# Kernel tuning notes

Measured on AMD Instinct MI355X. Metric: run time of the kernel, lower is better.

## Reference

```python
import jax, jax.numpy as jnp
import numpy as np

B, T, DQ, DM, D, F, K, WIN = 64, 2000, 1024, 512, 128, 32, 31, 7
NEG = -2.0**32 + 1.0

def setup_inputs() -> dict:
    key = jax.random.key(0)
    ks = jax.random.split(key, 12)
    return {
        "query": jax.random.normal(ks[0], (B, DQ), jnp.float32),
        "memory": jax.random.normal(ks[1], (B, T, DM), jnp.float32),
        "prev_alignments": jax.random.uniform(ks[2], (B, T), jnp.float32),
        "prev_max_attentions": jax.random.randint(ks[3], (B,), 0, T),
        "memory_lengths": jax.random.randint(ks[4], (B,), T // 2, T),
        "Wq": jax.random.normal(ks[5], (DQ, D), jnp.float32) * 0.02,
        "Wm": jax.random.normal(ks[6], (DM, D), jnp.float32) * 0.02,
        "conv_kernel": jax.random.normal(ks[7], (K, 1, F), jnp.float32) * 0.1,
        "conv_bias": jnp.zeros((F,), jnp.float32),
        "Wloc": jax.random.normal(ks[8], (F, D), jnp.float32) * 0.1,
        "score_v": jax.random.normal(ks[9], (D,), jnp.float32) * 0.1,
        "score_b": jnp.zeros((D,), jnp.float32),
    }

def reference(query, memory, prev_alignments, prev_max_attentions, memory_lengths,
              Wq, Wm, conv_kernel, conv_bias, Wloc, score_v, score_b):
    # projections
    pq = (query @ Wq)[:, None, :]                              # [B,1,D]
    values = jnp.einsum('btm,md->btd', memory, Wm)             # [B,T,D]
    # location features: Conv1D 'same' over prev alignments
    f = jax.lax.conv_general_dilated(
        prev_alignments[:, :, None], conv_kernel, (1,), 'SAME',
        dimension_numbers=('NWC', 'WIO', 'NWC')) + conv_bias    # [B,T,F]
    ploc = jnp.einsum('btf,fd->btd', f, Wloc)                  # [B,T,D]
    # additive energy
    energy = jnp.sum(score_v * jnp.tanh(values + pq + ploc + score_b), axis=2)  # [B,T]
    # monotonic window mask + length mask
    t_idx = jnp.arange(T)
    key_mask = t_idx[None, :] < prev_max_attentions[:, None]
    mask_lengths = jnp.maximum(0, T - WIN - prev_max_attentions)
    reverse_mask = (t_idx[None, :] < mask_lengths[:, None])[:, ::-1]
    length_mask = t_idx[None, :] < memory_lengths[:, None]
    mask = (~(key_mask | reverse_mask)) & length_mask
    energy = jnp.where(mask, energy, NEG)
    alignments = jax.nn.softmax(energy, axis=1)                # [B,T]
    max_attentions = jnp.argmax(alignments, axis=1)            # [B]
    attention = jnp.einsum('bt,btd->bd', alignments, values)   # [B,D]
    next_state = alignments + prev_alignments                  # cumulate_weight=True
    return attention, alignments, next_state, max_attentions
```

## Files before the change

### kernel.cpp

```cpp
#include <hip/hip_runtime.h>

#define B    64
#define T    2000
#define DQ   1024
#define DM   512
#define D    128
#define F    32
#define KK   31
#define WIN  7
#define NCH  32
#define CH   63
#define NCS  (B * NCH)
#define NPQ  (B * 4)

#define PQ4_OFF (NCS * DM)

#define OUT_ALIGN 8192
#define OUT_NEXT  (8192 + B*T)
#define OUT_ARG   (8192 + 2*B*T)

__global__ void __launch_bounds__(512)
K1(const float* __restrict__ q, const float* __restrict__ mem,
   const int* __restrict__ pm, const int* __restrict__ ml,
   const float* __restrict__ Wq, float* __restrict__ part,
   float* __restrict__ pq4) {
    __shared__ float red[4][D];
    int blk = blockIdx.x;
    int tid = threadIdx.x;

    if (blk < NCS) {
        int b = blk >> 5, c = blk & 31;
        if (pm[b] < ml[b]) return;
        int t0 = c * CH, t1 = t0 + CH;
        if (t1 > T) t1 = T;
        const float* mp = mem + ((size_t)b * T + t0) * DM + tid;
        float a0 = 0.f, a1 = 0.f, a2 = 0.f, a3 = 0.f;
        int t = t0;
        for (; t + 4 <= t1; t += 4) {
            a0 += mp[0];
            a1 += mp[DM];
            a2 += mp[2 * DM];
            a3 += mp[3 * DM];
            mp += 4 * (size_t)DM;
        }
        for (; t < t1; ++t) { a0 += *mp; mp += DM; }
        part[((size_t)b * NCH + c) * DM + tid] = ((a0 + a1) + (a2 + a3)) * (1.f / (float)T);
        return;
    }

    int s = blk - NCS;
    int b = s >> 2, j = s & 3;
    int d = tid & 127, kk = tid >> 7;
    int k0 = j * 256 + kk * 64;
    const float* qp = q + (size_t)b * DQ + k0;
    const float* wp = Wq + (size_t)k0 * D + d;
    float acc = 0.f;
    #pragma unroll 4
    for (int k = 0; k < 64; ++k)
        acc += qp[k] * wp[(size_t)k * D];
    red[kk][d] = acc;
    __syncthreads();
    if (tid < D)
        pq4[((size_t)b * 4 + j) * D + tid] =
            (red[0][tid] + red[1][tid]) + (red[2][tid] + red[3][tid]);
}

__global__ void __launch_bounds__(512)
K2(const float* __restrict__ q, const float* __restrict__ mem,
   const float* __restrict__ pa, const int* __restrict__ pm, const int* __restrict__ ml,
   const float* __restrict__ Wq, const float* __restrict__ Wm,
   const float* __restrict__ ck, const float* __restrict__ cb,
   const float* __restrict__ Wloc, const float* __restrict__ sv,
   const float* __restrict__ sb, const float* __restrict__ part,
   const float* __restrict__ pq4, float* __restrict__ out, int lowmem) {
    __shared__ __align__(16) float mrow[WIN][DM];
    __shared__ float fsh[WIN][F];
    __shared__ float2 pacc2[WIN][8][64];
    __shared__ float vsh[WIN][D];
    __shared__ float pqs[D];
    __shared__ float esh[WIN];
    __shared__ float ash[WIN];
    __shared__ int   sbest;

    int b = blockIdx.x;
    int tid = threadIdx.x;
    int lane = tid & 63;
    int wave = tid >> 6;
    int p = pm[b], L = ml[b];
    int wstart = p, wlen = 0;
    if (p < L) { int we = p + WIN; if (we > L) we = L; wlen = we - p; }

    if (wlen > 0) {
        for (int e = tid; e < WIN * DM; e += 512) {
            int i = e >> 9, m = e & 511;
            mrow[i][m] = (i < wlen) ? mem[((size_t)b * T + wstart + i) * DM + m] : 0.f;
        }
        if (tid < WIN * F) {
            int i = tid >> 5, f = tid & 31;
            if (i < wlen) {
                int t = wstart + i;
                float acc = cb[f];
                for (int k = 0; k < KK; ++k) {
                    int tt = t + k - 15;
                    float x = (tt >= 0 && tt < T) ? pa[(size_t)b * T + tt] : 0.f;
                    acc += x * ck[k * F + f];
                }
                fsh[i][f] = acc;
            } else if (i < WIN) {
                fsh[i][f] = 0.f;
            }
        }
        if (!lowmem) {
            if (tid < D) {
                const float* pp = pq4 + (size_t)b * 4 * D;
                pqs[tid] = (pp[tid] + pp[D + tid]) + (pp[2 * D + tid] + pp[3 * D + tid]) + sb[tid];
            }
        } else {
            int d = tid & 127, j = tid >> 7;
            int k0 = j * 256;
            const float* qp = q + (size_t)b * DQ + k0;
            float acc = 0.f;
            for (int k = 0; k < 256; ++k)
                acc += qp[k] * Wq[(size_t)(k0 + k) * D + d];
            ((float*)pacc2)[j * D + d] = acc;
            __syncthreads();
            if (tid < D) {
                const float* pp = (const float*)pacc2;
                pqs[tid] = (pp[tid] + pp[D + tid]) + (pp[2 * D + tid] + pp[3 * D + tid]) + sb[tid];
            }
        }
        __syncthreads();

        {
            const float2* Wm2 = (const float2*)Wm;
            float2 acc[WIN];
            #pragma unroll
            for (int i = 0; i < WIN; ++i) { acc[i].x = 0.f; acc[i].y = 0.f; }
            int m0 = wave * 64;
            for (int mm = 0; mm < 64; ++mm) {
                int m = m0 + mm;
                float2 wrow = Wm2[(size_t)m * 64 + lane];
                #pragma unroll
                for (int i = 0; i < WIN; ++i) {
                    float a = mrow[i][m];
                    acc[i].x += a * wrow.x;
                    acc[i].y += a * wrow.y;
                }
            }
            #pragma unroll
            for (int i = 0; i < WIN; ++i) pacc2[i][wave][lane] = acc[i];
        }
        __syncthreads();

        if (wave < wlen) {
            int i = wave;
            float2 s2 = {0.f, 0.f};
            #pragma unroll
            for (int w = 0; w < 8; ++w) {
                s2.x += pacc2[i][w][lane].x;
                s2.y += pacc2[i][w][lane].y;
            }
            ((float2*)vsh[i])[lane] = s2;
            const float2* Wl2 = (const float2*)Wloc;
            float p0 = 0.f, p1 = 0.f;
            #pragma unroll
            for (int f = 0; f < F; ++f) {
                float fv = fsh[i][f];
                float2 wv = Wl2[f * 64 + lane];
                p0 += fv * wv.x; p1 += fv * wv.y;
            }
            int c0 = 2 * lane, c1 = c0 + 1;
            float x = sv[c0] * tanhf(s2.x + pqs[c0] + p0)
                    + sv[c1] * tanhf(s2.y + pqs[c1] + p1);
            for (int o = 32; o > 0; o >>= 1) x += __shfl_xor(x, o);
            if (lane == 0) esh[i] = x;
        }
        __syncthreads();

        if (tid == 0) {
            float a[WIN];
            int best = 0;
            float mx = esh[0];
            for (int i = 1; i < wlen; ++i) if (esh[i] > mx) mx = esh[i];
            float s = 0.f;
            for (int i = 0; i < wlen; ++i) { a[i] = expf(esh[i] - mx); s += a[i]; }
            float inv = 1.f / s;
            float ab = -1.f;
            for (int i = 0; i < wlen; ++i) {
                a[i] *= inv;
                if (a[i] > ab) { ab = a[i]; best = i; }
            }
            for (int i = 0; i < WIN; ++i) ash[i] = (i < wlen) ? a[i] : 0.f;
            sbest = wstart + best;
        }
        __syncthreads();

        if (tid < D) {
            float a = 0.f;
            for (int i = 0; i < wlen; ++i) a += ash[i] * vsh[i][tid];
            out[b * D + tid] = a;
        }
    } else {
        float* ctxs = (float*)mrow;
        float* gpart = ((float*)mrow) + DM;
        if (!lowmem) {
            float s = 0.f;
            #pragma unroll 8
            for (int cc = 0; cc < NCH; ++cc)
                s += part[((size_t)b * NCH + cc) * DM + tid];
            ctxs[tid] = s;
        } else {
            const float* mp = mem + (size_t)b * T * DM + tid;
            float a0 = 0.f, a1 = 0.f, a2 = 0.f, a3 = 0.f;
            int t = 0;
            for (; t + 4 <= T; t += 4) {
                a0 += mp[0]; a1 += mp[DM]; a2 += mp[2 * DM]; a3 += mp[3 * DM];
                mp += 4 * (size_t)DM;
            }
            for (; t < T; ++t) { a0 += *mp; mp += DM; }
            ctxs[tid] = ((a0 + a1) + (a2 + a3)) * (1.f / (float)T);
        }
        __syncthreads();
        {
            int col = tid & 127, j = tid >> 7;
            const float* wp = Wm + (size_t)(j * 128) * D + col;
            float acc = 0.f;
            for (int mm = 0; mm < 128; ++mm)
                acc += ctxs[j * 128 + mm] * wp[(size_t)mm * D];
            gpart[j * D + col] = acc;
        }
        __syncthreads();
        if (tid < D)
            out[b * D + tid] = gpart[tid] + gpart[D + tid] + gpart[2 * D + tid] + gpart[3 * D + tid];
    }

    {
        float invT = 1.f / (float)T;
        for (int t = tid; t < T; t += 512) {
            float a;
            if (wlen == 0) a = invT;
            else a = (t >= wstart && t < wstart + wlen) ? ash[t - wstart] : 0.f;
            out[OUT_ALIGN + b * T + t] = a;
            out[OUT_NEXT + b * T + t] = pa[(size_t)b * T + t] + a;
        }
        if (tid == 0) out[OUT_ARG + b] = (float)((wlen > 0) ? sbest : 0);
    }
}

extern "C" void kernel_launch(void* const* d_in, const int* in_sizes, int n_in,
                              void* d_out, int out_size, void* d_ws, size_t ws_size,
                              hipStream_t stream) {
    const float* query = (const float*)d_in[0];
    const float* memory = (const float*)d_in[1];
    const float* prev_align = (const float*)d_in[2];
    const int* prev_max = (const int*)d_in[3];
    const int* mem_len = (const int*)d_in[4];
    const float* Wq = (const float*)d_in[5];
    const float* Wm = (const float*)d_in[6];
    const float* ck = (const float*)d_in[7];
    const float* cb = (const float*)d_in[8];
    const float* Wloc = (const float*)d_in[9];
    const float* sv = (const float*)d_in[10];
    const float* sb = (const float*)d_in[11];
    float* out = (float*)d_out;

    float* part = (float*)d_ws;
    float* pq4 = (float*)d_ws + PQ4_OFF;

    size_t need = (size_t)(NCS * DM + NPQ * D) * 4;
    int lowmem = (ws_size < need) ? 1 : 0;

    if (!lowmem)
        K1<<<NCS + NPQ, 512, 0, stream>>>(query, memory, prev_max, mem_len,
                                          Wq, part, pq4);
    K2<<<B, 512, 0, stream>>>(query, memory, prev_align, prev_max, mem_len,
                              Wq, Wm, ck, cb, Wloc, sv, sb,
                              part, pq4, out, lowmem);
}
```

Before: 30.95 us.

## Move window memory projection into first kernel to shorten serial second kernel

The 7-row window projection against Wm (memory rows times Wm) moves out of the per-batch K2 blocks into 64 extra K1 blocks. Each of those blocks writes per-wave partial sums to workspace, and K2 then sums them. The aim is to shorten K2, which runs only 64 blocks and serially loads memory rows and does the GEMV, by overlapping that work with the mean-reduction blocks already in K1. The low-workspace path is split into a separate K2L kernel. In exchange the change needs more workspace and adds global partial-sum traffic, and K1 also grows its shared memory, which may lower its occupancy.

Result: faster. 27.41 us (median of 2 runs) (-11.4%).

```diff
diff --git a/kernel.cpp b/kernel.cpp
--- a/kernel.cpp
+++ b/kernel.cpp
@@ -14,6 +14,7 @@
 #define NPQ  (B * 4)
 
 #define PQ4_OFF (NCS * DM)
+#define VP_OFF  (NCS * DM + NPQ * D)
 
 #define OUT_ALIGN 8192
 #define OUT_NEXT  (8192 + B*T)
@@ -22,9 +23,10 @@
 __global__ void __launch_bounds__(512)
 K1(const float* __restrict__ q, const float* __restrict__ mem,
    const int* __restrict__ pm, const int* __restrict__ ml,
-   const float* __restrict__ Wq, float* __restrict__ part,
-   float* __restrict__ pq4) {
+   const float* __restrict__ Wq, const float* __restrict__ Wm,
+   float* __restrict__ part, float* __restrict__ pq4, float* __restrict__ vpart) {
     __shared__ float red[4][D];
+    __shared__ __align__(16) float mrow[WIN][DM];
     int blk = blockIdx.x;
     int tid = threadIdx.x;
 
@@ -48,7 +50,40 @@
         return;
     }
 
-    int s = blk - NCS;
+    if (blk < NCS + B) {
+        int b = blk - NCS;
+        int p = pm[b], L = ml[b];
+        int wstart = p, wlen = 0;
+        if (p < L) { int we = p + WIN; if (we > L) we = L; wlen = we - p; }
+        if (wlen == 0) return;
+        for (int e = tid; e < WIN * DM; e += 512) {
+            int i = e >> 9, m = e & 511;
+            mrow[i][m] = (i < wlen) ? mem[((size_t)b * T + wstart + i) * DM + m] : 0.f;
+        }
+        __syncthreads();
+        int lane = tid & 63, wave = tid >> 6;
+        const float2* Wm2 = (const float2*)Wm;
+        float2 acc[WIN];
+        #pragma unroll
+        for (int i = 0; i < WIN; ++i) { acc[i].x = 0.f; acc[i].y = 0.f; }
+        int m0 = wave * 64;
+        for (int mm = 0; mm < 64; ++mm) {
+            int m = m0 + mm;
+            float2 wrow = Wm2[(size_t)m * 64 + lane];
+            #pragma unroll
+            for (int i = 0; i < WIN; ++i) {
+                float a = mrow[i][m];
+                acc[i].x += a * wrow.x;
+                acc[i].y += a * wrow.y;
+            }
+        }
+        float2* vp = (float2*)vpart + ((size_t)b * 8 + wave) * (WIN * 64);
+        #pragma unroll
+        for (int i = 0; i < WIN; ++i) vp[i * 64 + lane] = acc[i];
+        return;
+    }
+
+    int s = blk - NCS - B;
     int b = s >> 2, j = s & 3;
     int d = tid & 127, kk = tid >> 7;
     int k0 = j * 256 + kk * 64;
@@ -66,21 +101,18 @@
 }
 
 __global__ void __launch_bounds__(512)
-K2(const float* __restrict__ q, const float* __restrict__ mem,
-   const float* __restrict__ pa, const int* __restrict__ pm, const int* __restrict__ ml,
-   const float* __restrict__ Wq, const float* __restrict__ Wm,
-   const float* __restrict__ ck, const float* __restrict__ cb,
-   const float* __restrict__ Wloc, const float* __restrict__ sv,
-   const float* __restrict__ sb, const float* __restrict__ part,
-   const float* __restrict__ pq4, float* __restrict__ out, int lowmem) {
-    __shared__ __align__(16) float mrow[WIN][DM];
+K2(const float* __restrict__ pa, const int* __restrict__ pm, const int* __restrict__ ml,
+   const float* __restrict__ Wm, const float* __restrict__ ck, const float* __restrict__ cb,
+   const float* __restrict__ Wloc, const float* __restrict__ sv, const float* __restrict__ sb,
+   const float* __restrict__ part, const float* __restrict__ pq4,
+   const float* __restrict__ vpart, float* __restrict__ out) {
     __shared__ float fsh[WIN][F];
-    __shared__ float2 pacc2[WIN][8][64];
     __shared__ float vsh[WIN][D];
     __shared__ float pqs[D];
     __shared__ float esh[WIN];
     __shared__ float ash[WIN];
     __shared__ int   sbest;
+    __shared__ __align__(16) float cg[DM + 4 * D];
 
     int b = blockIdx.x;
     int tid = threadIdx.x;
@@ -91,10 +123,6 @@
     if (p < L) { int we = p + WIN; if (we > L) we = L; wlen = we - p; }
 
     if (wlen > 0) {
-        for (int e = tid; e < WIN * DM; e += 512) {
-            int i = e >> 9, m = e & 511;
-            mrow[i][m] = (i < wlen) ? mem[((size_t)b * T + wstart + i) * DM + m] : 0.f;
-        }
         if (tid < WIN * F) {
             int i = tid >> 5, f = tid & 31;
             if (i < wlen) {
@@ -110,55 +138,21 @@
                 fsh[i][f] = 0.f;
             }
         }
-        if (!lowmem) {
-            if (tid < D) {
-                const float* pp = pq4 + (size_t)b * 4 * D;
-                pqs[tid] = (pp[tid] + pp[D + tid]) + (pp[2 * D + tid] + pp[3 * D + tid]) + sb[tid];
-            }
-        } else {
-            int d = tid & 127, j = tid >> 7;
-            int k0 = j * 256;
-            const float* qp = q + (size_t)b * DQ + k0;
-            float acc = 0.f;
-            for (int k = 0; k < 256; ++k)
-                acc += qp[k] * Wq[(size_t)(k0 + k) * D + d];
-            ((float*)pacc2)[j * D + d] = acc;
-            __syncthreads();
-            if (tid < D) {
-                const float* pp = (const float*)pacc2;
-                pqs[tid] = (pp[tid] + pp[D + tid]) + (pp[2 * D + tid] + pp[3 * D + tid]) + sb[tid];
-            }
-        }
-        __syncthreads();
-
-        {
-            const float2* Wm2 = (const float2*)Wm;
-            float2 acc[WIN];
-            #pragma unroll
-            for (int i = 0; i < WIN; ++i) { acc[i].x = 0.f; acc[i].y = 0.f; }
-            int m0 = wave * 64;
-            for (int mm = 0; mm < 64; ++mm) {
-                int m = m0 + mm;
-                float2 wrow = Wm2[(size_t)m * 64 + lane];
-                #pragma unroll
-                for (int i = 0; i < WIN; ++i) {
-                    float a = mrow[i][m];
-                    acc[i].x += a * wrow.x;
-                    acc[i].y += a * wrow.y;
-                }
-            }
-            #pragma unroll
-            for (int i = 0; i < WIN; ++i) pacc2[i][wave][lane] = acc[i];
+        if (tid < D) {
+            const float* pp = pq4 + (size_t)b * 4 * D;
+            pqs[tid] = (pp[tid] + pp[D + tid]) + (pp[2 * D + tid] + pp[3 * D + tid]) + sb[tid];
         }
         __syncthreads();
 
         if (wave < wlen) {
             int i = wave;
+            const float2* vp = (const float2*)vpart + (size_t)b * 8 * (WIN * 64);
             float2 s2 = {0.f, 0.f};
             #pragma unroll
             for (int w = 0; w < 8; ++w) {
-                s2.x += pacc2[i][w][lane].x;
-                s2.y += pacc2[i][w][lane].y;
+                float2 v = vp[(size_t)w * (WIN * 64) + i * 64 + lane];
+                s2.x += v.x;
+                s2.y += v.y;
             }
             ((float2*)vsh[i])[lane] = s2;
             const float2* Wl2 = (const float2*)Wloc;
@@ -201,25 +195,177 @@
             out[b * D + tid] = a;
         }
     } else {
+        float* ctxs = cg;
+        float* gpart = cg + DM;
+        float s = 0.f;
+        #pragma unroll 8
+        for (int cc = 0; cc < NCH; ++cc)
+            s += part[((size_t)b * NCH + cc) * DM + tid];
+        ctxs[tid] = s;
+        __syncthreads();
+        {
+            int col = tid & 127, j = tid >> 7;
+            const float* wp = Wm + (size_t)(j * 128) * D + col;
+            float acc = 0.f;
+            for (int mm = 0; mm < 128; ++mm)
+                acc += ctxs[j * 128 + mm] * wp[(size_t)mm * D];
+            gpart[j * D + col] = acc;
+        }
+        __syncthreads();
+        if (tid < D)
+            out[b * D + tid] = gpart[tid] + gpart[D + tid] + gpart[2 * D + tid] + gpart[3 * D + tid];
+    }
+
+    {
+        float invT = 1.f / (float)T;
+        for (int t = tid; t < T; t += 512) {
+            float a;
+            if (wlen == 0) a = invT;
+            else a = (t >= wstart && t < wstart + wlen) ? ash[t - wstart] : 0.f;
+            out[OUT_ALIGN + b * T + t] = a;
+            out[OUT_NEXT + b * T + t] = pa[(size_t)b * T + t] + a;
+        }
+        if (tid == 0) out[OUT_ARG + b] = (float)((wlen > 0) ? sbest : 0);
+    }
+}
+
+__global__ void __launch_bounds__(512)
+K2L(const float* __restrict__ q, const float* __restrict__ mem,
+    const float* __restrict__ pa, const int* __restrict__ pm, const int* __restrict__ ml,
+    const float* __restrict__ Wq, const float* __restrict__ Wm,
+    const float* __restrict__ ck, const float* __restrict__ cb,
+    const float* __restrict__ Wloc, const float* __restrict__ sv,
+    const float* __restrict__ sb, float* __restrict__ out) {
+    __shared__ __align__(16) float mrow[WIN][DM];
+    __shared__ float fsh[WIN][F];
+    __shared__ float2 pacc2[WIN][8][64];
+    __shared__ float vsh[WIN][D];
+    __shared__ float pqs[D];
+    __shared__ float esh[WIN];
+    __shared__ float ash[WIN];
+    __shared__ int   sbest;
+
+    int b = blockIdx.x;
+    int tid = threadIdx.x;
+    int lane = tid & 63;
+    int wave = tid >> 6;
+    int p = pm[b], L = ml[b];
+    int wstart = p, wlen = 0;
+    if (p < L) { int we = p + WIN; if (we > L) we = L; wlen = we - p; }
+
+    if (wlen > 0) {
+        for (int e = tid; e < WIN * DM; e += 512) {
+            int i = e >> 9, m = e & 511;
+            mrow[i][m] = (i < wlen) ? mem[((size_t)b * T + wstart + i) * DM + m] : 0.f;
+        }
+        if (tid < WIN * F) {
+            int i = tid >> 5, f = tid & 31;
+            if (i < wlen) {
+                int t = wstart + i;
+                float acc = cb[f];
+                for (int k = 0; k < KK; ++k) {
+                    int tt = t + k - 15;
+                    float x = (tt >= 0 && tt < T) ? pa[(size_t)b * T + tt] : 0.f;
+                    acc += x * ck[k * F + f];
+                }
+                fsh[i][f] = acc;
+            } else if (i < WIN) {
+                fsh[i][f] = 0.f;
+            }
+        }
+        {
+            int d = tid & 127, j = tid >> 7;
+            int k0 = j * 256;
+            const float* qp = q + (size_t)b * DQ + k0;
+            float acc = 0.f;
+            for (int k = 0; k < 256; ++k)
+                acc += qp[k] * Wq[(size_t)(k0 + k) * D + d];
+            ((float*)pacc2)[j * D + d] = acc;
+            __syncthreads();
+            if (tid < D) {
+                const float* pp = (const float*)pacc2;
+                pqs[tid] = (pp[tid] + pp[D + tid]) + (pp[2 * D + tid] + pp[3 * D + tid]) + sb[tid];
+            }
+        }
+        __syncthreads();
+        {
+            const float2* Wm2 = (const float2*)Wm;
+            float2 acc[WIN];
+            #pragma unroll
+            for (int i = 0; i < WIN; ++i) { acc[i].x = 0.f; acc[i].y = 0.f; }
+            int m0 = wave * 64;
+            for (int mm = 0; mm < 64; ++mm) {
+                int m = m0 + mm;
+                float2 wrow = Wm2[(size_t)m * 64 + lane];
+                #pragma unroll
+                for (int i = 0; i < WIN; ++i) {
+                    float a = mrow[i][m];
+                    acc[i].x += a * wrow.x;
+                    acc[i].y += a * wrow.y;
+                }
+            }
+            #pragma unroll
+            for (int i = 0; i < WIN; ++i) pacc2[i][wave][lane] = acc[i];
+        }
+        __syncthreads();
+        if (wave < wlen) {
+            int i = wave;
+            float2 s2 = {0.f, 0.f};
+            #pragma unroll
+            for (int w = 0; w < 8; ++w) {
+                s2.x += pacc2[i][w][lane].x;
+                s2.y += pacc2[i][w][lane].y;
+            }
+            ((float2*)vsh[i])[lane] = s2;
+            const float2* Wl2 = (const float2*)Wloc;
+            float p0 = 0.f, p1 = 0.f;
+            #pragma unroll
+            for (int f = 0; f < F; ++f) {
+                float fv = fsh[i][f];
+                float2 wv = Wl2[f * 64 + lane];
+                p0 += fv * wv.x; p1 += fv * wv.y;
+            }
+            int c0 = 2 * lane, c1 = c0 + 1;
+            float x = sv[c0] * tanhf(s2.x + pqs[c0] + p0)
+                    + sv[c1] * tanhf(s2.y + pqs[c1] + p1);
+            for (int o = 32; o > 0; o >>= 1) x += __shfl_xor(x, o);
+            if (lane == 0) esh[i] = x;
+        }
+        __syncthreads();
+        if (tid == 0) {
+            float a[WIN];
+            int best = 0;
+            float mx = esh[0];
+            for (int i = 1; i < wlen; ++i) if (esh[i] > mx) mx = esh[i];
+            float s = 0.f;
+            for (int i = 0; i < wlen; ++i) { a[i] = expf(esh[i] - mx); s += a[i]; }
+            float inv = 1.f / s;
+            float ab = -1.f;
+            for (int i = 0; i < wlen; ++i) {
+                a[i] *= inv;
+                if (a[i] > ab) { ab = a[i]; best = i; }
+            }
+            for (int i = 0; i < WIN; ++i) ash[i] = (i < wlen) ? a[i] : 0.f;
+            sbest = wstart + best;
+        }
+        __syncthreads();
+        if (tid < D) {
+            float a = 0.f;
+            for (int i = 0; i < wlen; ++i) a += ash[i] * vsh[i][tid];
+            out[b * D + tid] = a;
+        }
+    } else {
         float* ctxs = (float*)mrow;
         float* gpart = ((float*)mrow) + DM;
-        if (!lowmem) {
-            float s = 0.f;
-            #pragma unroll 8
-            for (int cc = 0; cc < NCH; ++cc)
-                s += part[((size_t)b * NCH + cc) * DM + tid];
-            ctxs[tid] = s;
-        } else {
-            const float* mp = mem + (size_t)b * T * DM + tid;
-            float a0 = 0.f, a1 = 0.f, a2 = 0.f, a3 = 0.f;
-            int t = 0;
-            for (; t + 4 <= T; t += 4) {
-                a0 += mp[0]; a1 += mp[DM]; a2 += mp[2 * DM]; a3 += mp[3 * DM];
-                mp += 4 * (size_t)DM;
-            }
-            for (; t < T; ++t) { a0 += *mp; mp += DM; }
-            ctxs[tid] = ((a0 + a1) + (a2 + a3)) * (1.f / (float)T);
-        }
+        const float* mp = mem + (size_t)b * T * DM + tid;
+        float a0 = 0.f, a1 = 0.f, a2 = 0.f, a3 = 0.f;
+        int t = 0;
+        for (; t + 4 <= T; t += 4) {
+            a0 += mp[0]; a1 += mp[DM]; a2 += mp[2 * DM]; a3 += mp[3 * DM];
+            mp += 4 * (size_t)DM;
+        }
+        for (; t < T; ++t) { a0 += *mp; mp += DM; }
+        ctxs[tid] = ((a0 + a1) + (a2 + a3)) * (1.f / (float)T);
         __syncthreads();
         {
             int col = tid & 127, j = tid >> 7;
@@ -266,14 +412,18 @@
 
     float* part = (float*)d_ws;
     float* pq4 = (float*)d_ws + PQ4_OFF;
-
-    size_t need = (size_t)(NCS * DM + NPQ * D) * 4;
+    float* vpart = (float*)d_ws + VP_OFF;
+
+    size_t need = (size_t)(VP_OFF + B * 8 * WIN * 64 * 2) * 4;
     int lowmem = (ws_size < need) ? 1 : 0;
 
-    if (!lowmem)
-        K1<<<NCS + NPQ, 512, 0, stream>>>(query, memory, prev_max, mem_len,
-                                          Wq, part, pq4);
-    K2<<<B, 512, 0, stream>>>(query, memory, prev_align, prev_max, mem_len,
-                              Wq, Wm, ck, cb, Wloc, sv, sb,
-                              part, pq4, out, lowmem);
+    if (!lowmem) {
+        K1<<<NCS + B + NPQ, 512, 0, stream>>>(query, memory, prev_max, mem_len,
+                                              Wq, Wm, part, pq4, vpart);
+        K2<<<B, 512, 0, stream>>>(prev_align, prev_max, mem_len, Wm, ck, cb,
+                                  Wloc, sv, sb, part, pq4, vpart, out);
+    } else {
+        K2L<<<B, 512, 0, stream>>>(query, memory, prev_align, prev_max, mem_len,
+                                   Wq, Wm, ck, cb, Wloc, sv, sb, out);
+    }
 }
```
